# Optimization experiments

Hardware: AMD Instinct MI355X
Metric: run time of the kernel (lower is better)

Reference implementation:

```python
import jax, jax.numpy as jnp
import numpy as np

B, H, N, D = 2, 16, 4096, 128
SCALE = 1.0


def setup_inputs() -> dict:
    key = jax.random.key(0)
    kq, kk, kv, kg = jax.random.split(key, 4)
    shape = (B, H, N, D)
    return {
        "q": jax.random.normal(kq, shape, dtype=jnp.float32),
        "k": jax.random.normal(kk, shape, dtype=jnp.float32),
        "v": jax.random.normal(kv, shape, dtype=jnp.float32),
        "g": jax.random.normal(kg, shape, dtype=jnp.float32),
    }


def reference(q, k, v, g):
    # FLAOperator(mode='gla') CPU fallback: gla_scan
    # recurrence: s_t = s_{t-1} + sigmoid(q_t*k_t + g_t) * v_t ; y_t = s_t
    qs = q * SCALE
    # move time axis (N) to the front for lax.scan: [N, B, H, D]
    seq = tuple(jnp.moveaxis(t, 2, 0) for t in (qs, k, v, g))
    s0 = jnp.zeros((q.shape[0], q.shape[1], q.shape[3]), dtype=q.dtype)  # [B, H, D]

    def step(s, xs):
        q_t, k_t, v_t, g_t = xs
        s = s + jax.nn.sigmoid(q_t * k_t + g_t) * v_t
        return s, s

    _, y = jax.lax.scan(step, s0, seq)  # y: [N, B, H, D]
    return jnp.moveaxis(y, 0, 2)  # [B, H, N, D]
```

## Files before the change

### kernel.cpp

```cpp
#include <hip/hip_runtime.h>
#include <math.h>

static constexpr int kN   = 4096;
static constexpr int kD   = 128;
static constexpr int kBH  = 32;
static constexpr int kD4  = 32;

typedef float  v4f __attribute__((ext_vector_type(4)));

__device__ __forceinline__ float fast_sigmoid(float x) {
    return __builtin_amdgcn_rcpf(1.0f + __expf(-x));
}

__device__ __forceinline__ unsigned short f2b(float x) {
    union { float f; unsigned u; } cv; cv.f = x;
    unsigned u = cv.u;
    u += 0x7fffu + ((u >> 16) & 1u);
    return (unsigned short)(u >> 16);
}
__device__ __forceinline__ float b2f(unsigned short b) {
    union { unsigned u; float f; } cv; cv.u = ((unsigned)b) << 16;
    return cv.f;
}

static constexpr int C1 = 512;
static constexpr int T1 = kN / C1;
static constexpr int TASKS1 = kBH * C1;
static constexpr int M1 = 64;

__global__ __launch_bounds__(256) void gla1_scan(
    const float4* __restrict__ q, const float4* __restrict__ k,
    const float4* __restrict__ v, const float4* __restrict__ g,
    ushort4* __restrict__ wscan, float4* __restrict__ sums,
    float4* __restrict__ macros)
{
    __shared__ float4 lds[8][kD4];

    const int gtid = blockIdx.x * 256 + threadIdx.x;
    const int lane = gtid & (kD4 - 1);
    const int task = gtid >> 5;
    const int bh   = task >> 9;
    const int c    = task & (C1 - 1);
    const int grp  = threadIdx.x >> 5;

    const size_t base = ((size_t)bh * kN + (size_t)c * T1) * kD4 + lane;

    float4 acc = make_float4(0.f, 0.f, 0.f, 0.f);
#pragma unroll
    for (int t = 0; t < T1; ++t) {
        const size_t idx = base + (size_t)t * kD4;
        const float4 q4 = q[idx];
        const float4 k4 = k[idx];
        const float4 g4 = g[idx];
        const float4 v4 = v[idx];
        acc.x += v4.x * fast_sigmoid(q4.x * k4.x + g4.x);
        acc.y += v4.y * fast_sigmoid(q4.y * k4.y + g4.y);
        acc.z += v4.z * fast_sigmoid(q4.z * k4.z + g4.z);
        acc.w += v4.w * fast_sigmoid(q4.w * k4.w + g4.w);
        ushort4 p;
        p.x = f2b(acc.x); p.y = f2b(acc.y); p.z = f2b(acc.z); p.w = f2b(acc.w);
        wscan[idx] = p;
    }
    sums[(size_t)task * kD4 + lane] = acc;
    lds[grp][lane] = acc;
    __syncthreads();

    if (threadIdx.x < kD4) {
        float4 s = lds[0][threadIdx.x];
#pragma unroll
        for (int g2 = 1; g2 < 8; ++g2) {
            const float4 a = lds[g2][threadIdx.x];
            s.x += a.x; s.y += a.y; s.z += a.z; s.w += a.w;
        }
        macros[(size_t)blockIdx.x * kD4 + threadIdx.x] = s;
    }
}

__global__ void gla1_macroscan(float* __restrict__ M)
{
    const int bh = blockIdx.x;
    const int d  = threadIdx.x;
    const size_t base = (size_t)bh * M1 * kD + d;
    float run = 0.f;
    for (int m0 = 0; m0 < M1; m0 += 16) {
        float tv[16];
#pragma unroll
        for (int j = 0; j < 16; ++j)
            tv[j] = M[base + (size_t)(m0 + j) * kD];
#pragma unroll
        for (int j = 0; j < 16; ++j) {
            const float t = tv[j];
            M[base + (size_t)(m0 + j) * kD] = run;
            run += t;
        }
    }
}

__global__ __launch_bounds__(128) void gla1_chunkpre(
    float* __restrict__ S, const float* __restrict__ M)
{
    const int b  = blockIdx.x;
    const int d  = threadIdx.x;
    const int bh = b >> 6;
    const int m  = b & (M1 - 1);
    const size_t sbase = ((size_t)bh * C1 + (size_t)m * 8) * kD + d;

    float r[8];
#pragma unroll
    for (int j = 0; j < 8; ++j)
        r[j] = S[sbase + (size_t)j * kD];
    float pre = M[(size_t)b * kD + d];
#pragma unroll
    for (int j = 0; j < 8; ++j) {
        const float t = r[j];
        S[sbase + (size_t)j * kD] = pre;
        pre += t;
    }
}

__global__ __launch_bounds__(256) void gla1_emit(
    const ushort4* __restrict__ wscan, const float4* __restrict__ sums,
    float4* __restrict__ out)
{
    const int gtid = blockIdx.x * 256 + threadIdx.x;
    const int lane = gtid & (kD4 - 1);
    const int task = gtid >> 5;
    const int bh   = task >> 9;
    const int c    = task & (C1 - 1);

    const size_t base = ((size_t)bh * kN + (size_t)c * T1) * kD4 + lane;

    ushort4 p[T1];
#pragma unroll
    for (int t = 0; t < T1; ++t)
        p[t] = wscan[base + (size_t)t * kD4];
    const float4 pre = sums[(size_t)task * kD4 + lane];

#pragma unroll
    for (int t = 0; t < T1; ++t) {
        v4f o;
        o.x = b2f(p[t].x) + pre.x;
        o.y = b2f(p[t].y) + pre.y;
        o.z = b2f(p[t].z) + pre.z;
        o.w = b2f(p[t].w) + pre.w;
        __builtin_nontemporal_store(o, (v4f*)&out[base + (size_t)t * kD4]);
    }
}

template <int CC>
__global__ __launch_bounds__(256) void gla_pass1(
    const float4* __restrict__ q, const float4* __restrict__ k,
    const float4* __restrict__ v, const float4* __restrict__ g,
    float4* __restrict__ out, float4* __restrict__ sums)
{
    constexpr int TT = kN / CC;
    const int gtid = blockIdx.x * 256 + threadIdx.x;
    const int lane = gtid & (kD4 - 1);
    const int task = gtid >> 5;
    const int bh   = task / CC;
    const int c    = task & (CC - 1);
    size_t base = ((size_t)bh * kN + (size_t)c * TT) * kD4 + lane;
    float4 acc = make_float4(0.f, 0.f, 0.f, 0.f);
#pragma unroll 4
    for (int t = 0; t < TT; ++t) {
        const size_t idx = base + (size_t)t * kD4;
        const float4 q4 = q[idx], k4 = k[idx], g4 = g[idx], v4 = v[idx];
        acc.x += v4.x * fast_sigmoid(q4.x * k4.x + g4.x);
        acc.y += v4.y * fast_sigmoid(q4.y * k4.y + g4.y);
        acc.z += v4.z * fast_sigmoid(q4.z * k4.z + g4.z);
        acc.w += v4.w * fast_sigmoid(q4.w * k4.w + g4.w);
        out[idx] = acc;
    }
    sums[(size_t)task * kD4 + lane] = acc;
}

template <int CC>
__global__ void gla_pass2(float* __restrict__ sums)
{
    const int bh = blockIdx.x;
    const int d  = threadIdx.x;
    size_t base = (size_t)bh * CC * kD + d;
    float run = 0.f;
#pragma unroll
    for (int c2 = 0; c2 < CC; ++c2) {
        const size_t i = base + (size_t)c2 * kD;
        const float t = sums[i];
        sums[i] = run;
        run += t;
    }
}

template <int CC>
__global__ __launch_bounds__(256) void gla_pass3(
    float4* __restrict__ out, const float4* __restrict__ sums)
{
    constexpr int TT = kN / CC;
    const int gtid = blockIdx.x * 256 + threadIdx.x;
    const int lane = gtid & (kD4 - 1);
    const int nt   = gtid >> 5;
    const int bh   = nt / kN;
    const int t    = nt & (kN - 1);
    const int c    = t / TT;
    const float4 add = sums[((size_t)bh * CC + c) * kD4 + lane];
    float4 o = out[gtid];
    o.x += add.x; o.y += add.y; o.z += add.z; o.w += add.w;
    out[gtid] = o;
}

extern "C" void kernel_launch(void* const* d_in, const int* in_sizes, int n_in,
                              void* d_out, int out_size, void* d_ws,
                              size_t ws_size, hipStream_t stream)
{
    const float4* q = (const float4*)d_in[0];
    const float4* k = (const float4*)d_in[1];
    const float4* v = (const float4*)d_in[2];
    const float4* g = (const float4*)d_in[3];
    float4* out = (float4*)d_out;

    constexpr size_t kWscanBytes = (size_t)kBH * kN * kD4 * sizeof(ushort4);
    constexpr size_t kSumsBytes  = (size_t)TASKS1 * kD4 * sizeof(float4);
    constexpr size_t kMacroBytes = (size_t)kBH * M1 * kD4 * sizeof(float4);
    constexpr size_t kNeed1 = kWscanBytes + kSumsBytes + kMacroBytes;

    if (ws_size >= kNeed1) {
        ushort4* wscan = (ushort4*)d_ws;
        float4*  sums  = (float4*)((char*)d_ws + kWscanBytes);
        float4*  macros= (float4*)((char*)d_ws + kWscanBytes + kSumsBytes);
        const int blocks = TASKS1 * 32 / 256;
        gla1_scan<<<blocks, 256, 0, stream>>>(q, k, v, g, wscan, sums, macros);
        gla1_macroscan<<<kBH, kD, 0, stream>>>((float*)macros);
        gla1_chunkpre<<<kBH * M1, kD, 0, stream>>>((float*)sums,
                                                   (const float*)macros);
        gla1_emit<<<blocks, 256, 0, stream>>>(wscan, sums, out);
    } else if (ws_size >= (size_t)kBH * 128 * kD * sizeof(float)) {
        constexpr int CC = 128;
        const int threads1 = kBH * CC * 32;
        gla_pass1<CC><<<threads1 / 256, 256, 0, stream>>>(q, k, v, g, out,
                                                          (float4*)d_ws);
        gla_pass2<CC><<<kBH, kD, 0, stream>>>((float*)d_ws);
        const int threads3 = kBH * kN * kD4;
        gla_pass3<CC><<<threads3 / 256, 256, 0, stream>>>(out,
                                                          (const float4*)d_ws);
    } else {
        constexpr int CC = 32;
        const int threads1 = kBH * CC * 32;
        gla_pass1<CC><<<threads1 / 256, 256, 0, stream>>>(q, k, v, g, out,
                                                          (float4*)d_ws);
        gla_pass2<CC><<<kBH, kD, 0, stream>>>((float*)d_ws);
        const int threads3 = kBH * kN * kD4;
        gla_pass3<CC><<<threads3 / 256, 256, 0, stream>>>(out,
                                                          (const float4*)d_ws);
    }
}
```

Baseline: 76.39 us.

## Drop chunk-prefix kernel; recompute intra-block prefixes in emit from bf16 partials

Removes the per-chunk sums buffer and the chunkpre kernel. The emit kernel rebuilds each chunk's offset within its block by sharing the last bf16 partial of every group through LDS and adding it to the macro prefix. This cuts one launch and some global traffic, at the cost of using bf16-rounded chunk totals in the prefix, which lowers accuracy. Input loads in the scan kernel also become nontemporal.

```diff
diff --git a/kernel.cpp b/kernel.cpp
--- a/kernel.cpp
+++ b/kernel.cpp
@@ -6,7 +6,7 @@
 static constexpr int kBH  = 32;
 static constexpr int kD4  = 32;
 
-typedef float  v4f __attribute__((ext_vector_type(4)));
+typedef float v4f __attribute__((ext_vector_type(4)));
 
 __device__ __forceinline__ float fast_sigmoid(float x) {
     return __builtin_amdgcn_rcpf(1.0f + __expf(-x));
@@ -27,12 +27,12 @@
 static constexpr int T1 = kN / C1;
 static constexpr int TASKS1 = kBH * C1;
 static constexpr int M1 = 64;
+static constexpr int NBLK = kBH * M1;
 
 __global__ __launch_bounds__(256) void gla1_scan(
     const float4* __restrict__ q, const float4* __restrict__ k,
     const float4* __restrict__ v, const float4* __restrict__ g,
-    ushort4* __restrict__ wscan, float4* __restrict__ sums,
-    float4* __restrict__ macros)
+    ushort4* __restrict__ wscan, float4* __restrict__ macros)
 {
     __shared__ float4 lds[8][kD4];
 
@@ -49,10 +49,10 @@
 #pragma unroll
     for (int t = 0; t < T1; ++t) {
         const size_t idx = base + (size_t)t * kD4;
-        const float4 q4 = q[idx];
-        const float4 k4 = k[idx];
-        const float4 g4 = g[idx];
-        const float4 v4 = v[idx];
+        const v4f q4 = __builtin_nontemporal_load((const v4f*)&q[idx]);
+        const v4f k4 = __builtin_nontemporal_load((const v4f*)&k[idx]);
+        const v4f g4 = __builtin_nontemporal_load((const v4f*)&g[idx]);
+        const v4f v4 = __builtin_nontemporal_load((const v4f*)&v[idx]);
         acc.x += v4.x * fast_sigmoid(q4.x * k4.x + g4.x);
         acc.y += v4.y * fast_sigmoid(q4.y * k4.y + g4.y);
         acc.z += v4.z * fast_sigmoid(q4.z * k4.z + g4.z);
@@ -61,7 +61,6 @@
         p.x = f2b(acc.x); p.y = f2b(acc.y); p.z = f2b(acc.z); p.w = f2b(acc.w);
         wscan[idx] = p;
     }
-    sums[(size_t)task * kD4 + lane] = acc;
     lds[grp][lane] = acc;
     __syncthreads();
 
@@ -96,37 +95,18 @@
     }
 }
 
-__global__ __launch_bounds__(128) void gla1_chunkpre(
-    float* __restrict__ S, const float* __restrict__ M)
-{
-    const int b  = blockIdx.x;
-    const int d  = threadIdx.x;
-    const int bh = b >> 6;
-    const int m  = b & (M1 - 1);
-    const size_t sbase = ((size_t)bh * C1 + (size_t)m * 8) * kD + d;
-
-    float r[8];
-#pragma unroll
-    for (int j = 0; j < 8; ++j)
-        r[j] = S[sbase + (size_t)j * kD];
-    float pre = M[(size_t)b * kD + d];
-#pragma unroll
-    for (int j = 0; j < 8; ++j) {
-        const float t = r[j];
-        S[sbase + (size_t)j * kD] = pre;
-        pre += t;
-    }
-}
-
-__global__ __launch_bounds__(256) void gla1_emit(
-    const ushort4* __restrict__ wscan, const float4* __restrict__ sums,
+__global__ __launch_bounds__(256) void gla2_emit(
+    const ushort4* __restrict__ wscan, const float4* __restrict__ macros,
     float4* __restrict__ out)
 {
+    __shared__ float4 lds[8][kD4];
+
     const int gtid = blockIdx.x * 256 + threadIdx.x;
     const int lane = gtid & (kD4 - 1);
     const int task = gtid >> 5;
     const int bh   = task >> 9;
     const int c    = task & (C1 - 1);
+    const int grp  = threadIdx.x >> 5;
 
     const size_t base = ((size_t)bh * kN + (size_t)c * T1) * kD4 + lane;
 
@@ -134,7 +114,18 @@
 #pragma unroll
     for (int t = 0; t < T1; ++t)
         p[t] = wscan[base + (size_t)t * kD4];
-    const float4 pre = sums[(size_t)task * kD4 + lane];
+
+    const float4 tot = make_float4(b2f(p[T1-1].x), b2f(p[T1-1].y),
+                                   b2f(p[T1-1].z), b2f(p[T1-1].w));
+    lds[grp][lane] = tot;
+
+    float4 pre = macros[(size_t)blockIdx.x * kD4 + lane];
+    __syncthreads();
+
+    for (int g2 = 0; g2 < grp; ++g2) {
+        const float4 a = lds[g2][lane];
+        pre.x += a.x; pre.y += a.y; pre.z += a.z; pre.w += a.w;
+    }
 
 #pragma unroll
     for (int t = 0; t < T1; ++t) {
@@ -218,20 +209,15 @@
     float4* out = (float4*)d_out;
 
     constexpr size_t kWscanBytes = (size_t)kBH * kN * kD4 * sizeof(ushort4);
-    constexpr size_t kSumsBytes  = (size_t)TASKS1 * kD4 * sizeof(float4);
-    constexpr size_t kMacroBytes = (size_t)kBH * M1 * kD4 * sizeof(float4);
-    constexpr size_t kNeed1 = kWscanBytes + kSumsBytes + kMacroBytes;
+    constexpr size_t kMacroBytes = (size_t)NBLK * kD4 * sizeof(float4);
+    constexpr size_t kNeed1 = kWscanBytes + kMacroBytes;
 
     if (ws_size >= kNeed1) {
-        ushort4* wscan = (ushort4*)d_ws;
-        float4*  sums  = (float4*)((char*)d_ws + kWscanBytes);
-        float4*  macros= (float4*)((char*)d_ws + kWscanBytes + kSumsBytes);
-        const int blocks = TASKS1 * 32 / 256;
-        gla1_scan<<<blocks, 256, 0, stream>>>(q, k, v, g, wscan, sums, macros);
+        ushort4* wscan  = (ushort4*)d_ws;
+        float4*  macros = (float4*)((char*)d_ws + kWscanBytes);
+        gla1_scan<<<NBLK, 256, 0, stream>>>(q, k, v, g, wscan, macros);
         gla1_macroscan<<<kBH, kD, 0, stream>>>((float*)macros);
-        gla1_chunkpre<<<kBH * M1, kD, 0, stream>>>((float*)sums,
-                                                   (const float*)macros);
-        gla1_emit<<<blocks, 256, 0, stream>>>(wscan, sums, out);
+        gla2_emit<<<NBLK, 256, 0, stream>>>(wscan, macros, out);
     } else if (ws_size >= (size_t)kBH * 128 * kD * sizeof(float)) {
         constexpr int CC = 128;
         const int threads1 = kBH * CC * 32;
```

After: 73.47 us. -3.8%, faster.
